# Performance work log

Measured on AMD Instinct MI355X. Metric: run time of the kernel, lower is better.

Reference implementation:

```python
import jax, jax.numpy as jnp
import numpy as np

B, S, D, H = 4, 512, 1024, 16
HD = D // H
K_TOP = 8
MC_K = 8
EPS6 = 1e-6


def _affine(loc, scale, W, b):
    # Gaussian-diag affine: mu = x@W.T+b, var = scale^2 @ (W^2).T
    mu = loc @ W.T + b
    var = (scale ** 2) @ (W ** 2).T
    return mu, jnp.sqrt(var)


def _split(x):  # [B,S,D] -> [B,H,S,HD]
    return x.reshape(B, S, H, HD).transpose(0, 2, 1, 3)


def _combine(x):  # [B,H,S,HD] -> [B,S,D]
    return x.transpose(0, 2, 1, 3).reshape(B, S, D)


def _softmax_logit_normal(mu, var, excl_mask):
    # logit-normal softmax moment approximation (probit / delta method),
    # excluding masked positions (prob -> 0 there).
    adj = mu / jnp.sqrt(1.0 + (jnp.pi / 8.0) * var)
    adj = jnp.where(excl_mask, -1e9, adj)
    p = jax.nn.softmax(adj, axis=-1)
    v = (p * (1.0 - p)) ** 2 * var
    return p, v


def _forward(Q_loc, Q_scale, K_loc, K_scale, V_loc, V_scale,
             Wq, bq, Wk, bk, Wv, bv, Wo, bo, tau, eps):
    q_mu, q_sc = _affine(Q_loc, Q_scale, Wq, bq)
    k_mu, k_sc = _affine(K_loc, K_scale, Wk, bk)
    v_mu, v_sc = _affine(V_loc, V_scale, Wv, bv)

    # split heads; GaussianDiag round-trip adds 1e-6 to scale before squaring
    qm, qv = _split(q_mu), (_split(q_sc) + EPS6) ** 2
    km, kv = _split(k_mu), (_split(k_sc) + EPS6) ** 2
    vm, vv = _split(v_mu), (_split(v_sc) + EPS6) ** 2

    # bilinear moment: E[QK^T], Var[QK^T]
    S_mu = jnp.einsum('bhqd,bhkd->bhqk', qm, km)
    S_var = (jnp.einsum('bhqd,bhkd->bhqk', qm ** 2, kv)
             + jnp.einsum('bhqd,bhkd->bhqk', qv, km ** 2)
             + jnp.einsum('bhqd,bhkd->bhqk', qv, kv)) + EPS6

    s_mu = S_mu / jnp.sqrt(jnp.float32(HD))
    s_var = S_var / HD + EPS6

    l_mu = s_mu / tau
    l_var = s_var / (tau ** 2) + EPS6

    # top-k indices by mean logit
    topk_idx = jax.lax.top_k(l_mu, K_TOP)[1]  # [B,H,S,K_TOP]
    rows = jnp.arange(B * H * S)[:, None]
    mask = jnp.zeros((B * H * S, S), bool).at[rows, topk_idx.reshape(-1, K_TOP)].set(True)
    mask = mask.reshape(B, H, S, S)

    # MC-sample softmax (mc_k=8)
    std = jnp.sqrt(jnp.maximum(l_var, 1e-9))
    p_mean = jax.nn.softmax(l_mu[None] + std[None] * eps, axis=-1).mean(axis=0)

    # rest (non-top-k) logit-normal softmax moments
    rest_mean, rest_var = _softmax_logit_normal(l_mu, l_var, mask)

    top_out = jnp.where(mask, p_mean, rest_mean)
    top_out = top_out / jnp.maximum(top_out.sum(axis=-1, keepdims=True), 1e-12)

    # combine_top_rest: means add (variances do not feed the output path)
    attn_mu = top_out + rest_mean

    # linear combination with V distribution
    Y_mu = jnp.einsum('bhqk,bhkd->bhqd', attn_mu, vm)
    Y_var = jnp.einsum('bhqk,bhkd->bhqd', attn_mu ** 2, vv)
    Y_scale = jnp.sqrt(Y_var + EPS6)

    y_loc = _combine(Y_mu)
    y_scale = _combine(Y_scale) + EPS6

    out_loc = y_loc @ Wo.T + bo
    out_scale = jnp.sqrt((y_scale ** 2) @ (Wo ** 2).T)
    return out_loc, out_scale


def setup_inputs() -> dict:
    key = jax.random.key(0)
    ks = jax.random.split(key, 17)
    f32 = jnp.float32
    inp = {
        'Q_loc': jax.random.normal(ks[0], (B, S, D), f32),
        'Q_scale': jax.random.uniform(ks[1], (B, S, D), f32),
        'K_loc': jax.random.normal(ks[2], (B, S, D), f32),
        'K_scale': jax.random.uniform(ks[3], (B, S, D), f32),
        'V_loc': jax.random.normal(ks[4], (B, S, D), f32),
        'V_scale': jax.random.uniform(ks[5], (B, S, D), f32),
        'Wq': jax.random.normal(ks[6], (D, D), f32) * 0.02,
        'bq': jnp.zeros((D,), f32),
        'Wk': jax.random.normal(ks[7], (D, D), f32) * 0.02,
        'bk': jnp.zeros((D,), f32),
        'Wv': jax.random.normal(ks[8], (D, D), f32) * 0.02,
        'bv': jnp.zeros((D,), f32),
        'Wo': jax.random.normal(ks[9], (D, D), f32) * 0.02,
        'bo': jnp.zeros((D,), f32),
        'tau': jnp.array(1.0, f32),
        'eps': jax.random.normal(ks[10], (MC_K, B, H, S, S), f32),
    }
    return inp


def reference(Q_loc, Q_scale, K_loc, K_scale, V_loc, V_scale,
              Wq, bq, Wk, bk, Wv, bv, Wo, bo, tau, eps):
    return _forward(Q_loc, Q_scale, K_loc, K_scale, V_loc, V_scale,
                    Wq, bq, Wk, bk, Wv, bv, Wo, bo, tau, eps)
```

## Files before the change

### kernel.cpp

```cpp
#include <hip/hip_runtime.h>
#include <math.h>

#define B_ 4
#define S_ 512
#define D_ 1024
#define H_ 16
#define MCK 8
#define MS 2048
#define BHSS_ ((size_t)16777216)
#define BHS_  ((size_t)32768)

typedef __attribute__((ext_vector_type(8))) __bf16 bf16x8;
typedef __attribute__((ext_vector_type(4))) __bf16 bf16x4;
typedef __attribute__((ext_vector_type(4))) float f32x4;

__device__ __forceinline__ f32x4 mfma16(bf16x8 a, bf16x8 b, f32x4 c) {
  return __builtin_amdgcn_mfma_f32_16x16x32_bf16(a, b, c, 0, 0, 0);
}
__device__ __forceinline__ bf16x8 sq8(bf16x8 x) {
  bf16x8 r;
#pragma unroll
  for (int i = 0; i < 8; ++i) { float f = (float)x[i]; r[i] = (__bf16)(f * f); }
  return r;
}
__device__ __forceinline__ bf16x8 sq8s(bf16x8 h, bf16x8 l) {
  bf16x8 r;
#pragma unroll
  for (int i = 0; i < 8; ++i) { float f = (float)h[i] + (float)l[i]; r[i] = (__bf16)(f * f); }
  return r;
}
__device__ __forceinline__ float wave_max(float v) {
#pragma unroll
  for (int o = 32; o; o >>= 1) v = fmaxf(v, __shfl_xor(v, o));
  return v;
}
__device__ __forceinline__ float wave_sum(float v) {
#pragma unroll
  for (int o = 32; o; o >>= 1) v += __shfl_xor(v, o);
  return v;
}

__device__ __forceinline__ void unswz(int u, int& row, int& slot) {
  int row0 = ((u >> 2) ^ (u >> 4)) & 1;
  row = ((u >> 3) << 1) | row0;
  int s0 = (u ^ (u >> 2) ^ (u >> 4)) & 1;
  int s1 = ((u >> 1) ^ (u >> 3)) & 1;
  slot = (s1 << 1) | s0;
}
__device__ __forceinline__ int swz_el(int row, int slot) {
  return ((row * 4 + slot) ^ (row & 7)) * 8;
}
__device__ __forceinline__ void glds16(const void* gsrc, void* ldst) {
  __builtin_amdgcn_global_load_lds(
      (const __attribute__((address_space(1))) void*)gsrc,
      (__attribute__((address_space(3))) void*)ldst, 16, 0, 0);
}

__global__ __launch_bounds__(256) void conv_ls(
    const float* __restrict__ l0, const float* __restrict__ s0,
    const float* __restrict__ l1, const float* __restrict__ s1,
    const float* __restrict__ l2, const float* __restrict__ s2,
    __bf16* h0, __bf16* o0, __bf16* v0,
    __bf16* h1, __bf16* o1, __bf16* v1,
    __bf16* h2, __bf16* o2, __bf16* v2)
{
  const int tn = blockIdx.x >> 10;
  const size_t i0 = ((size_t)(blockIdx.x & 1023) * 256 + threadIdx.x) * 8;
  const float* L = tn == 0 ? l0 : tn == 1 ? l1 : l2;
  const float* S = tn == 0 ? s0 : tn == 1 ? s1 : s2;
  __bf16* Hh = tn == 0 ? h0 : tn == 1 ? h1 : h2;
  __bf16* Lo = tn == 0 ? o0 : tn == 1 ? o1 : o2;
  __bf16* V2 = tn == 0 ? v0 : tn == 1 ? v1 : v2;
  float4 x0 = *(const float4*)(L + i0), x1 = *(const float4*)(L + i0 + 4);
  float4 y0 = *(const float4*)(S + i0), y1 = *(const float4*)(S + i0 + 4);
  float xs[8] = {x0.x, x0.y, x0.z, x0.w, x1.x, x1.y, x1.z, x1.w};
  float ys[8] = {y0.x, y0.y, y0.z, y0.w, y1.x, y1.y, y1.z, y1.w};
  bf16x8 hh, ll, vv;
#pragma unroll
  for (int i = 0; i < 8; ++i) {
    __bf16 h = (__bf16)xs[i];
    hh[i] = h;
    ll[i] = (__bf16)(xs[i] - (float)h);
    vv[i] = (__bf16)(ys[i] * ys[i]);
  }
  *(bf16x8*)(Hh + i0) = hh;
  *(bf16x8*)(Lo + i0) = ll;
  *(bf16x8*)(V2 + i0) = vv;
}

__global__ __launch_bounds__(256) void conv_w(
    const float* __restrict__ w0, const float* __restrict__ w1,
    const float* __restrict__ w2, const float* __restrict__ w3,
    __bf16* h0, __bf16* o0, __bf16* h1, __bf16* o1,
    __bf16* h2, __bf16* o2, __bf16* h3, __bf16* o3)
{
  const int tn = blockIdx.x >> 9;
  const size_t i0 = ((size_t)(blockIdx.x & 511) * 256 + threadIdx.x) * 8;
  const float* W = tn == 0 ? w0 : tn == 1 ? w1 : tn == 2 ? w2 : w3;
  __bf16* Hh = tn == 0 ? h0 : tn == 1 ? h1 : tn == 2 ? h2 : h3;
  __bf16* Lo = tn == 0 ? o0 : tn == 1 ? o1 : tn == 2 ? o2 : o3;
  float4 x0 = *(const float4*)(W + i0), x1 = *(const float4*)(W + i0 + 4);
  float xs[8] = {x0.x, x0.y, x0.z, x0.w, x1.x, x1.y, x1.z, x1.w};
  bf16x8 hh, ll;
#pragma unroll
  for (int i = 0; i < 8; ++i) {
    __bf16 h = (__bf16)xs[i];
    hh[i] = h;
    ll[i] = (__bf16)(xs[i] - (float)h);
  }
  *(bf16x8*)(Hh + i0) = hh;
  *(bf16x8*)(Lo + i0) = ll;
}

struct PArg {
  const __bf16 *Ah, *Al, *A2, *Wh, *Wl;
  const float* bias;
  __bf16 *P0, *P1, *P2, *P3;
  int epi;
};
struct PArg3 { PArg a[3]; };

__global__ __launch_bounds__(256, 3) void dgemm_qkv(PArg3 P3v)
{
  __shared__ __bf16 lds[14336];
  const PArg p = P3v.a[blockIdx.z];
  const int t = threadIdx.x, lane = t & 63, wid = t >> 6;
  const int m0 = blockIdx.y * 64, n0 = blockIdx.x * 128;
  int rA, sA; unswz(t, rA, sA);
  const size_t gA = (size_t)(m0 + rA) * D_ + sA * 8;
  const size_t gW0 = (size_t)(n0 + rA) * D_ + sA * 8;
  int rW1, sW1; unswz(t + 256, rW1, sW1);
  const size_t gW1 = (size_t)(n0 + rW1) * D_ + sW1 * 8;
  const int wofs = wid * 512;
  f32x4 accM[4][2] = {}; f32x4 accV[4][2] = {};
  const int fr = lane & 15, ks = lane >> 4;
  for (int k0 = 0; k0 < D_; k0 += 32) {
    if (k0) __syncthreads();
    glds16(p.Ah + gA + k0,  lds + 0     + wofs);
    glds16(p.Al + gA + k0,  lds + 2048  + wofs);
    glds16(p.A2 + gA + k0,  lds + 4096  + wofs);
    glds16(p.Wh + gW0 + k0, lds + 6144  + wofs);
    glds16(p.Wl + gW0 + k0, lds + 10240 + wofs);
    glds16(p.Wh + gW1 + k0, lds + 6144 + 2048 + wofs);
    glds16(p.Wl + gW1 + k0, lds + 10240 + 2048 + wofs);
    __syncthreads();
    bf16x8 fah[4], fal[4], fa2[4];
#pragma unroll
    for (int i = 0; i < 4; ++i) {
      int so = swz_el(i * 16 + fr, ks);
      fah[i] = *(const bf16x8*)(lds + 0 + so);
      fal[i] = *(const bf16x8*)(lds + 2048 + so);
      fa2[i] = *(const bf16x8*)(lds + 4096 + so);
    }
#pragma unroll
    for (int j = 0; j < 2; ++j) {
      int so = swz_el(wid * 32 + j * 16 + fr, ks);
      bf16x8 fwh = *(const bf16x8*)(lds + 6144 + so);
      bf16x8 fwl = *(const bf16x8*)(lds + 10240 + so);
      bf16x8 fw2 = sq8s(fwh, fwl);
#pragma unroll
      for (int i = 0; i < 4; ++i) {
        accM[i][j] = mfma16(fah[i], fwh, accM[i][j]);
        accM[i][j] = mfma16(fah[i], fwl, accM[i][j]);
        accM[i][j] = mfma16(fal[i], fwh, accM[i][j]);
        accV[i][j] = mfma16(fa2[i], fw2, accV[i][j]);
      }
    }
  }
  const int fq = lane >> 4;
#pragma unroll
  for (int j = 0; j < 2; ++j) {
    const int col = n0 + wid * 32 + j * 16 + fr;
    const float bcol = p.bias[col];
#pragma unroll
    for (int i = 0; i < 4; ++i) {
      const int row0 = m0 + i * 16 + fq * 4;
      f32x4 m_ = accM[i][j], v_ = accV[i][j];
      if (p.epi == 0) {
#pragma unroll
        for (int r = 0; r < 4; ++r) {
          size_t off = (size_t)(row0 + r) * D_ + col;
          float mu = m_[r] + bcol;
          __bf16 h = (__bf16)mu;
          float s = sqrtf(v_[r]) + 1e-6f;
          p.P0[off] = h;
          p.P1[off] = (__bf16)(mu - (float)h);
          p.P2[off] = (__bf16)(mu * mu);
          p.P3[off] = (__bf16)(s * s);
        }
      } else {
        const int b = row0 >> 9, ss0 = row0 & 511;
        const int hh = col >> 6, dd = col & 63;
        size_t base = ((size_t)(b * H_ + hh) * 64 + dd) * S_ + ss0;
        bf16x4 vh, vl, vq;
#pragma unroll
        for (int r = 0; r < 4; ++r) {
          float mu = m_[r] + bcol;
          __bf16 h = (__bf16)mu;
          vh[r] = h;
          vl[r] = (__bf16)(mu - (float)h);
          float s = sqrtf(v_[r]) + 1e-6f;
          vq[r] = (__bf16)(s * s);
        }
        *(bf16x4*)(p.P0 + base) = vh;
        *(bf16x4*)(p.P1 + base) = vl;
        *(bf16x4*)(p.P2 + base) = vq;
      }
    }
  }
}

__global__ __launch_bounds__(256) void dgemm_o(
    const __bf16* __restrict__ Ah, const __bf16* __restrict__ Al, const __bf16* __restrict__ A2,
    const __bf16* __restrict__ Wh, const __bf16* __restrict__ Wl,
    const float* __restrict__ bias, float* __restrict__ O0, float* __restrict__ O1)
{
  __shared__ __bf16 lds[14336];
  const int t = threadIdx.x, lane = t & 63, wid = t >> 6;
  const int m0 = blockIdx.y * 64, n0 = blockIdx.x * 128;
  int rA, sA; unswz(t, rA, sA);
  const size_t gA = (size_t)(m0 + rA) * D_ + sA * 8;
  const size_t gW0 = (size_t)(n0 + rA) * D_ + sA * 8;
  int rW1, sW1; unswz(t + 256, rW1, sW1);
  const size_t gW1 = (size_t)(n0 + rW1) * D_ + sW1 * 8;
  const int wofs = wid * 512;
  f32x4 accM[4][2] = {}; f32x4 accV[4][2] = {};
  const int fr = lane & 15, ks = lane >> 4;
  for (int k0 = 0; k0 < D_; k0 += 32) {
    if (k0) __syncthreads();
    glds16(Ah + gA + k0,  lds + 0     + wofs);
    glds16(Al + gA + k0,  lds + 2048  + wofs);
    glds16(A2 + gA + k0,  lds + 4096  + wofs);
    glds16(Wh + gW0 + k0, lds + 6144  + wofs);
    glds16(Wl + gW0 + k0, lds + 10240 + wofs);
    glds16(Wh + gW1 + k0, lds + 6144 + 2048 + wofs);
    glds16(Wl + gW1 + k0, lds + 10240 + 2048 + wofs);
    __syncthreads();
    bf16x8 fah[4], fal[4], fa2[4];
#pragma unroll
    for (int i = 0; i < 4; ++i) {
      int so = swz_el(i * 16 + fr, ks);
      fah[i] = *(const bf16x8*)(lds + 0 + so);
      fal[i] = *(const bf16x8*)(lds + 2048 + so);
      fa2[i] = *(const bf16x8*)(lds + 4096 + so);
    }
#pragma unroll
    for (int j = 0; j < 2; ++j) {
      int so = swz_el(wid * 32 + j * 16 + fr, ks);
      bf16x8 fwh = *(const bf16x8*)(lds + 6144 + so);
      bf16x8 fwl = *(const bf16x8*)(lds + 10240 + so);
      bf16x8 fw2 = sq8s(fwh, fwl);
#pragma unroll
      for (int i = 0; i < 4; ++i) {
        accM[i][j] = mfma16(fah[i], fwh, accM[i][j]);
        accM[i][j] = mfma16(fah[i], fwl, accM[i][j]);
        accM[i][j] = mfma16(fal[i], fwh, accM[i][j]);
        accV[i][j] = mfma16(fa2[i], fw2, accV[i][j]);
      }
    }
  }
  const int fq = lane >> 4;
#pragma unroll
  for (int j = 0; j < 2; ++j) {
    const int col = n0 + wid * 32 + j * 16 + fr;
    const float bcol = bias[col];
#pragma unroll
    for (int i = 0; i < 4; ++i) {
      const int row0 = m0 + i * 16 + fq * 4;
      f32x4 m_ = accM[i][j], v_ = accV[i][j];
#pragma unroll
      for (int r = 0; r < 4; ++r) {
        size_t off = (size_t)(row0 + r) * D_ + col;
        O0[off] = m_[r] + bcol;
        O1[off] = sqrtf(v_[r]);
      }
    }
  }
}

__global__ __launch_bounds__(256) void score_mfma(
    const __bf16* __restrict__ qh, const __bf16* __restrict__ ql,
    const __bf16* __restrict__ q2, const __bf16* __restrict__ qv,
    const __bf16* __restrict__ kh, const __bf16* __restrict__ kl,
    const __bf16* __restrict__ k2, const __bf16* __restrict__ kv,
    float* __restrict__ lmu, __bf16* __restrict__ lvar,
    const float* __restrict__ taup)
{
  __shared__ __bf16 sQ[4][64][32];
  __shared__ __bf16 sK[4][64][32];
  const int t = threadIdx.x;
  const int lane = t & 63, wid = t >> 6;
  const int wm = wid >> 1, wn = wid & 1;
  const int kk0 = blockIdx.x * 64, q0 = blockIdx.y * 64, bh = blockIdx.z;
  const int b = bh >> 4, h = bh & 15;
  const size_t hb = ((size_t)b * S_) * D_ + (size_t)h * 64;
  f32x4 accM[2][2] = {}; f32x4 accV[2][2] = {};
  const int crow = t >> 2, ccol = (t & 3) * 8;
  for (int d0 = 0; d0 < 64; d0 += 32) {
    size_t gq = hb + (size_t)(q0 + crow) * D_ + d0 + ccol;
    size_t gk = hb + (size_t)(kk0 + crow) * D_ + d0 + ccol;
    bf16x8 a0 = *(const bf16x8*)(qh + gq);
    bf16x8 a1 = *(const bf16x8*)(ql + gq);
    bf16x8 a2 = *(const bf16x8*)(q2 + gq);
    bf16x8 a3 = *(const bf16x8*)(qv + gq);
    bf16x8 b0 = *(const bf16x8*)(kh + gk);
    bf16x8 b1 = *(const bf16x8*)(kl + gk);
    bf16x8 b2 = *(const bf16x8*)(k2 + gk);
    bf16x8 b3 = *(const bf16x8*)(kv + gk);
    __syncthreads();
    *(bf16x8*)&sQ[0][crow][ccol] = a0;
    *(bf16x8*)&sQ[1][crow][ccol] = a1;
    *(bf16x8*)&sQ[2][crow][ccol] = a2;
    *(bf16x8*)&sQ[3][crow][ccol] = a3;
    *(bf16x8*)&sK[0][crow][ccol] = b0;
    *(bf16x8*)&sK[1][crow][ccol] = b1;
    *(bf16x8*)&sK[2][crow][ccol] = b2;
    *(bf16x8*)&sK[3][crow][ccol] = b3;
    __syncthreads();
    const int fr = lane & 15, kc = (lane >> 4) * 8;
    bf16x8 fqh[2], fql[2], fq2[2], fqv[2];
#pragma unroll
    for (int i = 0; i < 2; ++i) {
      int r = wm * 32 + i * 16 + fr;
      fqh[i] = *(const bf16x8*)&sQ[0][r][kc];
      fql[i] = *(const bf16x8*)&sQ[1][r][kc];
      fq2[i] = *(const bf16x8*)&sQ[2][r][kc];
      fqv[i] = *(const bf16x8*)&sQ[3][r][kc];
    }
#pragma unroll
    for (int j = 0; j < 2; ++j) {
      int r = wn * 32 + j * 16 + fr;
      bf16x8 fkh = *(const bf16x8*)&sK[0][r][kc];
      bf16x8 fkl = *(const bf16x8*)&sK[1][r][kc];
      bf16x8 fk2 = *(const bf16x8*)&sK[2][r][kc];
      bf16x8 fkv = *(const bf16x8*)&sK[3][r][kc];
#pragma unroll
      for (int i = 0; i < 2; ++i) {
        accM[i][j] = mfma16(fqh[i], fkh, accM[i][j]);
        accM[i][j] = mfma16(fqh[i], fkl, accM[i][j]);
        accM[i][j] = mfma16(fql[i], fkh, accM[i][j]);
        accV[i][j] = mfma16(fq2[i], fkv, accV[i][j]);
        accV[i][j] = mfma16(fqv[i], fk2, accV[i][j]);
        accV[i][j] = mfma16(fqv[i], fkv, accV[i][j]);
      }
    }
  }
  const float itau = 1.0f / *taup;
  const int fr = lane & 15, fq = lane >> 4;
#pragma unroll
  for (int i = 0; i < 2; ++i)
#pragma unroll
    for (int j = 0; j < 2; ++j) {
      const int col = kk0 + wn * 32 + j * 16 + fr;
      const int row0 = q0 + wm * 32 + i * 16 + fq * 4;
      f32x4 m_ = accM[i][j], v_ = accV[i][j];
#pragma unroll
      for (int r = 0; r < 4; ++r) {
        size_t off = ((size_t)bh * S_ + row0 + r) * S_ + col;
        lmu[off] = m_[r] * 0.125f * itau;
        float lv = ((v_[r] + 1e-6f) * (1.0f / 64.0f) + 1e-6f) * itau * itau + 1e-6f;
        lvar[off] = (__bf16)lv;
      }
    }
}

__global__ __launch_bounds__(256) void attn_kernel(
    const float* __restrict__ lmu, const __bf16* __restrict__ lvar,
    const float* __restrict__ eps, __bf16* __restrict__ ah, __bf16* __restrict__ al)
{
  const int wid = threadIdx.x >> 6;
  const int lane = threadIdx.x & 63;
  const size_t r = (size_t)blockIdx.x * 4 + wid;
  const float* mrow = lmu + r * S_;
  const __bf16* vrow = lvar + r * S_;
  const int c0 = lane * 4;
  float mu[8], va[8], sd[8];
  {
    float4 m0 = *(const float4*)(mrow + c0);
    float4 m1 = *(const float4*)(mrow + 256 + c0);
    mu[0] = m0.x; mu[1] = m0.y; mu[2] = m0.z; mu[3] = m0.w;
    mu[4] = m1.x; mu[5] = m1.y; mu[6] = m1.z; mu[7] = m1.w;
    bf16x4 v0 = *(const bf16x4*)(vrow + c0);
    bf16x4 v1 = *(const bf16x4*)(vrow + 256 + c0);
#pragma unroll
    for (int i = 0; i < 4; ++i) { va[i] = (float)v0[i]; va[4 + i] = (float)v1[i]; }
  }
#pragma unroll
  for (int i = 0; i < 8; ++i) sd[i] = sqrtf(fmaxf(va[i], 1e-9f));
  unsigned sel = 0;
  float x[8];
#pragma unroll
  for (int i = 0; i < 8; ++i) x[i] = mu[i];
  for (int tsel = 0; tsel < 8; ++tsel) {
    float bv = -INFINITY; int bi = 0x7fffffff;
#pragma unroll
    for (int i = 0; i < 8; ++i) {
      int gi = (i < 4) ? (c0 + i) : (256 + c0 + i - 4);
      if (x[i] > bv || (x[i] == bv && gi < bi)) { bv = x[i]; bi = gi; }
    }
    for (int o = 32; o; o >>= 1) {
      float ov = __shfl_xor(bv, o); int oi = __shfl_xor(bi, o);
      if (ov > bv || (ov == bv && oi < bi)) { bv = ov; bi = oi; }
    }
    int half = bi >> 8;
    int rem = bi & 255;
    if ((rem >> 2) == lane) {
      int slot = (rem & 3) + 4 * half;
      sel |= 1u << slot;
      x[slot] = -INFINITY;
    }
  }
  float pacc[8] = {0, 0, 0, 0, 0, 0, 0, 0};
  for (int mc = 0; mc < MCK; ++mc) {
    const float* ep = eps + (size_t)mc * BHSS_ + r * S_;
    float4 e0 = *(const float4*)(ep + c0);
    float4 e1 = *(const float4*)(ep + 256 + c0);
    float xv[8];
    xv[0] = mu[0] + sd[0] * e0.x; xv[1] = mu[1] + sd[1] * e0.y;
    xv[2] = mu[2] + sd[2] * e0.z; xv[3] = mu[3] + sd[3] * e0.w;
    xv[4] = mu[4] + sd[4] * e1.x; xv[5] = mu[5] + sd[5] * e1.y;
    xv[6] = mu[6] + sd[6] * e1.z; xv[7] = mu[7] + sd[7] * e1.w;
    float m = -INFINITY;
#pragma unroll
    for (int i = 0; i < 8; ++i) m = fmaxf(m, xv[i]);
    m = wave_max(m);
    float e[8], zs = 0.f;
#pragma unroll
    for (int i = 0; i < 8; ++i) { e[i] = __expf(xv[i] - m); zs += e[i]; }
    zs = wave_sum(zs);
    float inv = 1.0f / zs;
#pragma unroll
    for (int i = 0; i < 8; ++i) pacc[i] += e[i] * inv;
  }
  float adj[8];
#pragma unroll
  for (int i = 0; i < 8; ++i) {
    float a = mu[i] / sqrtf(1.0f + 0.39269908169872414f * va[i]);
    adj[i] = ((sel >> i) & 1u) ? -1e9f : a;
  }
  float m2 = -INFINITY;
#pragma unroll
  for (int i = 0; i < 8; ++i) m2 = fmaxf(m2, adj[i]);
  m2 = wave_max(m2);
  float e2[8], z2 = 0.f;
#pragma unroll
  for (int i = 0; i < 8; ++i) { e2[i] = __expf(adj[i] - m2); z2 += e2[i]; }
  z2 = wave_sum(z2);
  float inv2 = 1.0f / z2;
  float rest[8], tout[8], s = 0.f;
#pragma unroll
  for (int i = 0; i < 8; ++i) {
    rest[i] = e2[i] * inv2;
    tout[i] = ((sel >> i) & 1u) ? pacc[i] * 0.125f : rest[i];
    s += tout[i];
  }
  s = wave_sum(s);
  float rn = 1.0f / fmaxf(s, 1e-12f);
  bf16x4 oh0, oh1, ol0, ol1;
#pragma unroll
  for (int i = 0; i < 4; ++i) {
    float o = tout[i] * rn + rest[i];
    __bf16 h = (__bf16)o;
    oh0[i] = h; ol0[i] = (__bf16)(o - (float)h);
    float o1 = tout[4 + i] * rn + rest[4 + i];
    __bf16 h1 = (__bf16)o1;
    oh1[i] = h1; ol1[i] = (__bf16)(o1 - (float)h1);
  }
  *(bf16x4*)(ah + r * S_ + c0) = oh0;
  *(bf16x4*)(ah + r * S_ + 256 + c0) = oh1;
  *(bf16x4*)(al + r * S_ + c0) = ol0;
  *(bf16x4*)(al + r * S_ + 256 + c0) = ol1;
}

__global__ __launch_bounds__(256) void pv_mfma(
    const __bf16* __restrict__ ah_, const __bf16* __restrict__ al_,
    const __bf16* __restrict__ vTh, const __bf16* __restrict__ vTl,
    const __bf16* __restrict__ vTv,
    __bf16* __restrict__ yh, __bf16* __restrict__ yl, __bf16* __restrict__ ys2)
{
  __shared__ __bf16 sA[2][64][32];
  __shared__ __bf16 sV[3][64][32];
  const int t = threadIdx.x;
  const int lane = t & 63, wid = t >> 6;
  const int wm = wid >> 1, wn = wid & 1;
  const int q0 = blockIdx.x * 64, bh = blockIdx.y;
  const int b = bh >> 4, h = bh & 15;
  const __bf16* Ah = ah_ + (size_t)bh * S_ * S_;
  const __bf16* Al = al_ + (size_t)bh * S_ * S_;
  const __bf16* Vh = vTh + (size_t)bh * 64 * S_;
  const __bf16* Vl = vTl + (size_t)bh * 64 * S_;
  const __bf16* Vv = vTv + (size_t)bh * 64 * S_;
  f32x4 accM[2][2] = {}; f32x4 accV[2][2] = {};
  const int crow = t >> 2, ccol = (t & 3) * 8;
  for (int k0 = 0; k0 < S_; k0 += 32) {
    size_t gA = (size_t)(q0 + crow) * S_ + k0 + ccol;
    size_t gV = (size_t)crow * S_ + k0 + ccol;
    bf16x8 a0 = *(const bf16x8*)(Ah + gA);
    bf16x8 a1 = *(const bf16x8*)(Al + gA);
    bf16x8 v0 = *(const bf16x8*)(Vh + gV);
    bf16x8 v1 = *(const bf16x8*)(Vl + gV);
    bf16x8 v2 = *(const bf16x8*)(Vv + gV);
    __syncthreads();
    *(bf16x8*)&sA[0][crow][ccol] = a0;
    *(bf16x8*)&sA[1][crow][ccol] = a1;
    *(bf16x8*)&sV[0][crow][ccol] = v0;
    *(bf16x8*)&sV[1][crow][ccol] = v1;
    *(bf16x8*)&sV[2][crow][ccol] = v2;
    __syncthreads();
    const int fr = lane & 15, kc = (lane >> 4) * 8;
    bf16x8 fah[2], fal[2], fa2[2];
#pragma unroll
    for (int i = 0; i < 2; ++i) {
      int rr = wm * 32 + i * 16 + fr;
      fah[i] = *(const bf16x8*)&sA[0][rr][kc];
      fal[i] = *(const bf16x8*)&sA[1][rr][kc];
      fa2[i] = sq8(fah[i]);
    }
#pragma unroll
    for (int j = 0; j < 2; ++j) {
      int rr = wn * 32 + j * 16 + fr;
      bf16x8 fvh = *(const bf16x8*)&sV[0][rr][kc];
      bf16x8 fvl = *(const bf16x8*)&sV[1][rr][kc];
      bf16x8 fvv = *(const bf16x8*)&sV[2][rr][kc];
#pragma unroll
      for (int i = 0; i < 2; ++i) {
        accM[i][j] = mfma16(fah[i], fvh, accM[i][j]);
        accM[i][j] = mfma16(fah[i], fvl, accM[i][j]);
        accM[i][j] = mfma16(fal[i], fvh, accM[i][j]);
        accV[i][j] = mfma16(fa2[i], fvv, accV[i][j]);
      }
    }
  }
  const int fr = lane & 15, fq = lane >> 4;
#pragma unroll
  for (int i = 0; i < 2; ++i)
#pragma unroll
    for (int j = 0; j < 2; ++j) {
      const int col = h * 64 + wn * 32 + j * 16 + fr;
      const int row0 = b * S_ + q0 + wm * 32 + i * 16 + fq * 4;
      f32x4 m_ = accM[i][j], v_ = accV[i][j];
#pragma unroll
      for (int r = 0; r < 4; ++r) {
        size_t off = (size_t)(row0 + r) * D_ + col;
        float mu = m_[r];
        __bf16 hh = (__bf16)mu;
        float ss = sqrtf(v_[r] + 1e-6f) + 1e-6f;
        yh[off] = hh;
        yl[off] = (__bf16)(mu - (float)hh);
        ys2[off] = (__bf16)(ss * ss);
      }
    }
}

extern "C" void kernel_launch(void* const* d_in, const int* in_sizes, int n_in,
                              void* d_out, int out_size, void* d_ws, size_t ws_size,
                              hipStream_t stream)
{
  const float* Qloc = (const float*)d_in[0];
  const float* Qsc  = (const float*)d_in[1];
  const float* Kloc = (const float*)d_in[2];
  const float* Ksc  = (const float*)d_in[3];
  const float* Vloc = (const float*)d_in[4];
  const float* Vsc  = (const float*)d_in[5];
  const float* Wq = (const float*)d_in[6];  const float* bq = (const float*)d_in[7];
  const float* Wk = (const float*)d_in[8];  const float* bk = (const float*)d_in[9];
  const float* Wv = (const float*)d_in[10]; const float* bv = (const float*)d_in[11];
  const float* Wo = (const float*)d_in[12]; const float* bo = (const float*)d_in[13];
  const float* tau = (const float*)d_in[14];
  const float* eps = (const float*)d_in[15];

  const size_t P = (size_t)MS * D_;
  const size_t DD = (size_t)D_ * D_;
  char* w = (char*)d_ws;
  auto carve = [&](size_t bytes) -> char* {
    char* p = w; w += (bytes + 255) & ~(size_t)255; return p;
  };
  __bf16* cQh = (__bf16*)carve(P * 2); __bf16* cQl = (__bf16*)carve(P * 2); __bf16* cQ2 = (__bf16*)carve(P * 2);
  __bf16* cKh = (__bf16*)carve(P * 2); __bf16* cKl = (__bf16*)carve(P * 2); __bf16* cK2 = (__bf16*)carve(P * 2);
  __bf16* cVh = (__bf16*)carve(P * 2); __bf16* cVl = (__bf16*)carve(P * 2); __bf16* cV2 = (__bf16*)carve(P * 2);
  __bf16* wqh = (__bf16*)carve(DD * 2); __bf16* wql = (__bf16*)carve(DD * 2);
  __bf16* wkh = (__bf16*)carve(DD * 2); __bf16* wkl = (__bf16*)carve(DD * 2);
  __bf16* wvh = (__bf16*)carve(DD * 2); __bf16* wvl = (__bf16*)carve(DD * 2);
  __bf16* woh = (__bf16*)carve(DD * 2); __bf16* wol = (__bf16*)carve(DD * 2);
  __bf16* qmh = (__bf16*)carve(P * 2); __bf16* qml = (__bf16*)carve(P * 2);
  __bf16* qm2 = (__bf16*)carve(P * 2); __bf16* qmv = (__bf16*)carve(P * 2);
  __bf16* kmh = (__bf16*)carve(P * 2); __bf16* kml = (__bf16*)carve(P * 2);
  __bf16* km2 = (__bf16*)carve(P * 2); __bf16* kmv = (__bf16*)carve(P * 2);
  __bf16* vTh = (__bf16*)carve(P * 2); __bf16* vTl = (__bf16*)carve(P * 2); __bf16* vTv = (__bf16*)carve(P * 2);
  float*  lmu = (float*)carve(BHSS_ * 4);
  __bf16* lvr = (__bf16*)carve(BHSS_ * 2);
  __bf16* ath = (__bf16*)carve(BHSS_ * 2);
  __bf16* atl = (__bf16*)carve(BHSS_ * 2);
  __bf16* yh = (__bf16*)carve(P * 2); __bf16* yl = (__bf16*)carve(P * 2); __bf16* ys2 = (__bf16*)carve(P * 2);
  float* out_loc = (float*)d_out;
  float* out_sc  = out_loc + P;

  dim3 blk(256);
  conv_ls<<<3 * 1024, blk, 0, stream>>>(Qloc, Qsc, Kloc, Ksc, Vloc, Vsc,
                                        cQh, cQl, cQ2, cKh, cKl, cK2, cVh, cVl, cV2);
  conv_w<<<4 * 512, blk, 0, stream>>>(Wq, Wk, Wv, Wo,
                                      wqh, wql, wkh, wkl, wvh, wvl, woh, wol);
  PArg3 pq;
  pq.a[0] = PArg{cQh, cQl, cQ2, wqh, wql, bq, qmh, qml, qm2, qmv, 0};
  pq.a[1] = PArg{cKh, cKl, cK2, wkh, wkl, bk, kmh, kml, km2, kmv, 0};
  pq.a[2] = PArg{cVh, cVl, cV2, wvh, wvl, bv, vTh, vTl, vTv, nullptr, 1};
  dgemm_qkv<<<dim3(8, 32, 3), blk, 0, stream>>>(pq);
  score_mfma<<<dim3(8, 8, 64), blk, 0, stream>>>(qmh, qml, qm2, qmv, kmh, kml, km2, kmv, lmu, lvr, tau);
  attn_kernel<<<dim3((unsigned)(BHS_ / 4)), blk, 0, stream>>>(lmu, lvr, eps, ath, atl);
  pv_mfma<<<dim3(8, 64), blk, 0, stream>>>(ath, atl, vTh, vTl, vTv, yh, yl, ys2);
  dgemm_o<<<dim3(8, 32), blk, 0, stream>>>(yh, yl, ys2, woh, wol, bo, out_loc, out_sc);
}
```

Baseline: 390.3 us.

## Double-buffer LDS in the split-precision projection GEMMs to overlap loads with MFMA

Both the QKV and output projection GEMM kernels now use two LDS buffers. The next K-slice is prefetched with global-to-LDS loads while MFMAs run on the current slice, and explicit vmcnt waits plus raw barriers replace __syncthreads. This is meant to hide global load latency that the old single-buffer loop exposed. In exchange it doubles LDS use and lowers the launch-bounds occupancy hint (QKV from 3 to 2 blocks, output GEMM gains an explicit 2), and it depends on the hand-counted vmcnt(7) matching the seven loads issued per stage.

```diff
diff --git a/kernel.cpp b/kernel.cpp
--- a/kernel.cpp
+++ b/kernel.cpp
@@ -120,9 +120,11 @@
 };
 struct PArg3 { PArg a[3]; };
 
-__global__ __launch_bounds__(256, 3) void dgemm_qkv(PArg3 P3v)
-{
-  __shared__ __bf16 lds[14336];
+#define LDSBUF 14336
+
+__global__ __launch_bounds__(256, 2) void dgemm_qkv(PArg3 P3v)
+{
+  __shared__ __bf16 lds[2 * LDSBUF];
   const PArg p = P3v.a[blockIdx.z];
   const int t = threadIdx.x, lane = t & 63, wid = t >> 6;
   const int m0 = blockIdx.y * 64, n0 = blockIdx.x * 128;
@@ -134,29 +136,43 @@
   const int wofs = wid * 512;
   f32x4 accM[4][2] = {}; f32x4 accV[4][2] = {};
   const int fr = lane & 15, ks = lane >> 4;
-  for (int k0 = 0; k0 < D_; k0 += 32) {
-    if (k0) __syncthreads();
-    glds16(p.Ah + gA + k0,  lds + 0     + wofs);
-    glds16(p.Al + gA + k0,  lds + 2048  + wofs);
-    glds16(p.A2 + gA + k0,  lds + 4096  + wofs);
-    glds16(p.Wh + gW0 + k0, lds + 6144  + wofs);
-    glds16(p.Wl + gW0 + k0, lds + 10240 + wofs);
-    glds16(p.Wh + gW1 + k0, lds + 6144 + 2048 + wofs);
-    glds16(p.Wl + gW1 + k0, lds + 10240 + 2048 + wofs);
-    __syncthreads();
+
+  auto STAGE = [&](int buf, int k0) {
+    __bf16* L = lds + buf * LDSBUF;
+    glds16(p.Ah + gA + k0,  L + 0     + wofs);
+    glds16(p.Al + gA + k0,  L + 2048  + wofs);
+    glds16(p.A2 + gA + k0,  L + 4096  + wofs);
+    glds16(p.Wh + gW0 + k0, L + 6144  + wofs);
+    glds16(p.Wl + gW0 + k0, L + 10240 + wofs);
+    glds16(p.Wh + gW1 + k0, L + 6144 + 2048 + wofs);
+    glds16(p.Wl + gW1 + k0, L + 10240 + 2048 + wofs);
+  };
+
+  STAGE(0, 0);
+  for (int tt = 0; tt < 32; ++tt) {
+    const int cur = tt & 1;
+    if (tt < 31) {
+      STAGE(cur ^ 1, (tt + 1) * 32);
+      asm volatile("s_waitcnt vmcnt(7)" ::: "memory");
+    } else {
+      asm volatile("s_waitcnt vmcnt(0)" ::: "memory");
+    }
+    __builtin_amdgcn_s_barrier();
+    __builtin_amdgcn_sched_barrier(0);
+    const __bf16* L = lds + cur * LDSBUF;
     bf16x8 fah[4], fal[4], fa2[4];
 #pragma unroll
     for (int i = 0; i < 4; ++i) {
       int so = swz_el(i * 16 + fr, ks);
-      fah[i] = *(const bf16x8*)(lds + 0 + so);
-      fal[i] = *(const bf16x8*)(lds + 2048 + so);
-      fa2[i] = *(const bf16x8*)(lds + 4096 + so);
+      fah[i] = *(const bf16x8*)(L + 0 + so);
+      fal[i] = *(const bf16x8*)(L + 2048 + so);
+      fa2[i] = *(const bf16x8*)(L + 4096 + so);
     }
 #pragma unroll
     for (int j = 0; j < 2; ++j) {
       int so = swz_el(wid * 32 + j * 16 + fr, ks);
-      bf16x8 fwh = *(const bf16x8*)(lds + 6144 + so);
-      bf16x8 fwl = *(const bf16x8*)(lds + 10240 + so);
+      bf16x8 fwh = *(const bf16x8*)(L + 6144 + so);
+      bf16x8 fwl = *(const bf16x8*)(L + 10240 + so);
       bf16x8 fw2 = sq8s(fwh, fwl);
 #pragma unroll
       for (int i = 0; i < 4; ++i) {
@@ -166,6 +182,7 @@
         accV[i][j] = mfma16(fa2[i], fw2, accV[i][j]);
       }
     }
+    __builtin_amdgcn_s_barrier();
   }
   const int fq = lane >> 4;
 #pragma unroll
@@ -210,12 +227,12 @@
   }
 }
 
-__global__ __launch_bounds__(256) void dgemm_o(
+__global__ __launch_bounds__(256, 2) void dgemm_o(
     const __bf16* __restrict__ Ah, const __bf16* __restrict__ Al, const __bf16* __restrict__ A2,
     const __bf16* __restrict__ Wh, const __bf16* __restrict__ Wl,
     const float* __restrict__ bias, float* __restrict__ O0, float* __restrict__ O1)
 {
-  __shared__ __bf16 lds[14336];
+  __shared__ __bf16 lds[2 * LDSBUF];
   const int t = threadIdx.x, lane = t & 63, wid = t >> 6;
   const int m0 = blockIdx.y * 64, n0 = blockIdx.x * 128;
   int rA, sA; unswz(t, rA, sA);
@@ -226,29 +243,43 @@
   const int wofs = wid * 512;
   f32x4 accM[4][2] = {}; f32x4 accV[4][2] = {};
   const int fr = lane & 15, ks = lane >> 4;
-  for (int k0 = 0; k0 < D_; k0 += 32) {
-    if (k0) __syncthreads();
-    glds16(Ah + gA + k0,  lds + 0     + wofs);
-    glds16(Al + gA + k0,  lds + 2048  + wofs);
-    glds16(A2 + gA + k0,  lds + 4096  + wofs);
-    glds16(Wh + gW0 + k0, lds + 6144  + wofs);
-    glds16(Wl + gW0 + k0, lds + 10240 + wofs);
-    glds16(Wh + gW1 + k0, lds + 6144 + 2048 + wofs);
-    glds16(Wl + gW1 + k0, lds + 10240 + 2048 + wofs);
-    __syncthreads();
+
+  auto STAGE = [&](int buf, int k0) {
+    __bf16* L = lds + buf * LDSBUF;
+    glds16(Ah + gA + k0,  L + 0     + wofs);
+    glds16(Al + gA + k0,  L + 2048  + wofs);
+    glds16(A2 + gA + k0,  L + 4096  + wofs);
+    glds16(Wh + gW0 + k0, L + 6144  + wofs);
+    glds16(Wl + gW0 + k0, L + 10240 + wofs);
+    glds16(Wh + gW1 + k0, L + 6144 + 2048 + wofs);
+    glds16(Wl + gW1 + k0, L + 10240 + 2048 + wofs);
+  };
+
+  STAGE(0, 0);
+  for (int tt = 0; tt < 32; ++tt) {
+    const int cur = tt & 1;
+    if (tt < 31) {
+      STAGE(cur ^ 1, (tt + 1) * 32);
+      asm volatile("s_waitcnt vmcnt(7)" ::: "memory");
+    } else {
+      asm volatile("s_waitcnt vmcnt(0)" ::: "memory");
+    }
+    __builtin_amdgcn_s_barrier();
+    __builtin_amdgcn_sched_barrier(0);
+    const __bf16* L = lds + cur * LDSBUF;
     bf16x8 fah[4], fal[4], fa2[4];
 #pragma unroll
     for (int i = 0; i < 4; ++i) {
       int so = swz_el(i * 16 + fr, ks);
-      fah[i] = *(const bf16x8*)(lds + 0 + so);
-      fal[i] = *(const bf16x8*)(lds + 2048 + so);
-      fa2[i] = *(const bf16x8*)(lds + 4096 + so);
+      fah[i] = *(const bf16x8*)(L + 0 + so);
+      fal[i] = *(const bf16x8*)(L + 2048 + so);
+      fa2[i] = *(const bf16x8*)(L + 4096 + so);
     }
 #pragma unroll
     for (int j = 0; j < 2; ++j) {
       int so = swz_el(wid * 32 + j * 16 + fr, ks);
-      bf16x8 fwh = *(const bf16x8*)(lds + 6144 + so);
-      bf16x8 fwl = *(const bf16x8*)(lds + 10240 + so);
+      bf16x8 fwh = *(const bf16x8*)(L + 6144 + so);
+      bf16x8 fwl = *(const bf16x8*)(L + 10240 + so);
       bf16x8 fw2 = sq8s(fwh, fwl);
 #pragma unroll
       for (int i = 0; i < 4; ++i) {
@@ -258,6 +289,7 @@
         accV[i][j] = mfma16(fa2[i], fw2, accV[i][j]);
       }
     }
+    __builtin_amdgcn_s_barrier();
   }
   const int fq = lane >> 4;
 #pragma unroll
```

After: 380.7 us. -2.5%, faster.
